# Optimization experiments

Hardware: AMD Instinct MI355X
Metric: run time of the kernel (lower is better)

Reference implementation:

```python
import jax, jax.numpy as jnp
import numpy as np

B, CIN, H, W = 4, 128, 128, 128
CH = CIN // 2          # channels after transpose conv (= 64)
COUT = 64
N2 = (B * 2 * H * 2 * W) // 2  # active sites of x2 (half of fine grid)


def setup_inputs() -> dict:
    key = jax.random.key(0)
    ks = jax.random.split(key, 8)
    n = lambda k, s, sc=1.0: jax.random.normal(k, s, jnp.float32) * sc
    return {
        "x1": n(ks[0], (B, CIN, H, W)),
        "x2_feat": n(ks[1], (N2, CH)),
        "w_up": n(ks[2], (CIN, CH, 2, 2), 0.05),   # torch ConvTranspose2d layout [in, out, kh, kw]
        "b_up": n(ks[3], (CH,), 0.05),
        "w1": n(ks[4], (CH, CH, 3, 3), 0.05),      # torch Conv2d layout [out, in, kh, kw]
        "b1": n(ks[5], (CH,), 0.05),
        "a1": jnp.full((1,), 0.25, jnp.float32),   # nn.PReLU default init
        "w2": n(ks[6], (COUT, CH, 3, 3), 0.05),
        "b2": n(ks[7], (COUT,), 0.05),
        "a2": jnp.full((1,), 0.25, jnp.float32),
    }


def _prelu(x, a):
    return jnp.where(x >= 0, x, a * x)


def _conv3(x, w, b):
    y = jax.lax.conv_general_dilated(x, w, (1, 1), 'SAME',
                                     dimension_numbers=('NCHW', 'OIHW', 'NCHW'))
    return y + b[None, :, None, None]


def reference(x1, x2_feat, w_up, b_up, w1, b1, a1, w2, b2, a2):
    Bn, _, Hn, Wn = x1.shape
    # ConvTranspose2d k=2, s=2 (non-overlapping) as an einsum:
    # up[b,o,2i+p,2j+q] = sum_c x1[b,c,i,j] * w_up[c,o,p,q]
    up = jnp.einsum('bchw,copq->bohpwq', x1, w_up).reshape(Bn, CH, 2 * Hn, 2 * Wn)
    up = up + b_up[None, :, None, None]
    # addspvec: larger tensor keeps its indices; first len(b) feature rows
    # are overwritten by the smaller tensor's features (spconv raster order).
    f = jnp.transpose(up, (0, 2, 3, 1)).reshape(-1, CH)  # [B*2H*2W, CH]
    f = f.at[:x2_feat.shape[0]].set(x2_feat)
    merged = jnp.transpose(f.reshape(Bn, 2 * Hn, 2 * Wn, CH), (0, 3, 1, 2))
    # DoubleConv: (SparseConv2d 3x3 pad1 -> PReLU) x 2 (dense-equivalent)
    h = _prelu(_conv3(merged, w1, b1), a1[0])
    out = _prelu(_conv3(h, w2, b2), a2[0])
    return out
```

## Files before the change

kernel.cpp:

```cpp
#include <hip/hip_runtime.h>

typedef __attribute__((ext_vector_type(8))) short short8;
typedef __attribute__((ext_vector_type(4))) float f32x4;

#define HF 256
#define WF 256

typedef const __attribute__((address_space(1))) void gbl_void;
typedef __attribute__((address_space(3))) void lds_void;

__device__ __forceinline__ ushort f2bf(float f) {
    uint u = __builtin_bit_cast(uint, f);
    u = (u + 0x7FFFu + ((u >> 16) & 1u)) >> 16;
    return (ushort)u;
}
__device__ __forceinline__ uint pack2(float a, float b) {
    return (uint)f2bf(a) | ((uint)f2bf(b) << 16);
}
__device__ __forceinline__ float prelu(float v, float al) { return v >= 0.f ? v : al * v; }

__global__ __launch_bounds__(256) void k_wprep(const float* __restrict__ w1,
                                               const float* __restrict__ w2,
                                               ushort* __restrict__ wT1,
                                               ushort* __restrict__ wT2,
                                               uint4* __restrict__ zeroBuf) {
    if (blockIdx.x == 0 && threadIdx.x < 16)
        zeroBuf[threadIdx.x] = make_uint4(0u, 0u, 0u, 0u);
    int idx = blockIdx.x * 256 + threadIdx.x;
    int tap = idx >> 12;
    int oc  = idx & 4095;
    int src = oc * 9 + tap;
    wT1[idx] = f2bf(w1[src]);
    wT2[idx] = f2bf(w2[src]);
}

__global__ __launch_bounds__(256) void k_wprep_up(const float* __restrict__ wup,
                                                  ushort* __restrict__ wupT) {
    int idx = blockIdx.x * 256 + threadIdx.x;
    int out = idx >> 7;
    int c   = idx & 127;
    int k   = out >> 6;
    int o   = out & 63;
    wupT[idx] = f2bf(wup[c * 256 + o * 4 + k]);
}

__global__ __launch_bounds__(512) void k_upsample_mfma(const float* __restrict__ x1,
                                                       const ushort* __restrict__ wupT,
                                                       const float* __restrict__ bup,
                                                       ushort* __restrict__ upB) {
    __shared__ __align__(16) char lds[81920];

    const int t   = threadIdx.x;
    const int l   = t & 63;
    const int l15 = l & 15;
    const int l4  = l >> 4;
    const int w   = t >> 6;
    const int pg  = w & 3;
    const int oh  = w >> 2;
    const int i   = blockIdx.x >> 1;
    const int j0  = (blockIdx.x & 1) * 64;
    const int z   = blockIdx.y;
    const int gb  = 2 + z;

    {
        const int j  = t & 63;
        const int cg = t >> 6;
        const size_t base = ((size_t)gb * 128) * 16384 + (size_t)i * 128 + j0 + j;
        float xv[16];
#pragma unroll
        for (int r = 0; r < 2; ++r)
#pragma unroll
            for (int cc = 0; cc < 8; ++cc)
                xv[r * 8 + cc] = x1[base + (size_t)(cg * 16 + r * 8 + cc) * 16384];
#pragma unroll
        for (int r = 0; r < 2; ++r) {
            short8 pk;
#pragma unroll
            for (int cc = 0; cc < 8; ++cc) pk[cc] = (short)f2bf(xv[r * 8 + cc]);
            int ad = (j * 256 + (cg * 16 + r * 8) * 2) ^ ((j & 15) << 4);
            *(short8*)(lds + ad) = pk;
        }
    }
    {
        const uint4* src = (const uint4*)wupT;
#pragma unroll
        for (int rep = 0; rep < 8; ++rep) {
            int q   = rep * 512 + t;
            int out = q >> 4, c16 = q & 15;
            int ad  = 16384 + ((out * 256 + c16 * 16) ^ ((out & 15) << 4));
            *(uint4*)(lds + ad) = src[q];
        }
    }
    float bvv[4];
#pragma unroll
    for (int ob = 0; ob < 4; ++ob) bvv[ob] = bup[ob * 16 + l15];
    __syncthreads();

    f32x4 acc[2][4];
#pragma unroll
    for (int kk = 0; kk < 2; ++kk)
#pragma unroll
        for (int ob = 0; ob < 4; ++ob) acc[kk][ob] = (f32x4){0.f, 0.f, 0.f, 0.f};

#pragma unroll
    for (int ks = 0; ks < 4; ++ks) {
        const int cb = ks * 64 + (l4 << 4);
        const int rowA = pg * 16 + l15;
        short8 xfr = *(const short8*)(lds + ((rowA * 256 + cb) ^ ((rowA & 15) << 4)));
#pragma unroll
        for (int kk = 0; kk < 2; ++kk)
#pragma unroll
            for (int ob = 0; ob < 4; ++ob) {
                int out = (oh * 2 + kk) * 64 + ob * 16 + l15;
                short8 wfr = *(const short8*)(lds + 16384 +
                              ((out * 256 + cb) ^ ((out & 15) << 4)));
                acc[kk][ob] = __builtin_amdgcn_mfma_f32_16x16x32_bf16(xfr, wfr, acc[kk][ob], 0, 0, 0);
            }
    }
    __syncthreads();

    ushort* OUT = (ushort*)lds;
#pragma unroll
    for (int kk = 0; kk < 2; ++kk) {
        const int k = oh * 2 + kk, p = k >> 1, q = k & 1;
#pragma unroll
        for (int ob = 0; ob < 4; ++ob) {
            const int o = ob * 16 + l15;
#pragma unroll
            for (int r = 0; r < 4; ++r) {
                int jl = pg * 16 + l4 * 4 + r;
                int x  = 2 * jl + q;
                OUT[(p * 128 + x) * 64 + o] = f2bf(acc[kk][ob][r] + bvv[ob]);
            }
        }
    }
    __syncthreads();

#pragma unroll
    for (int rep = 0; rep < 4; ++rep) {
        int idx = rep * 512 + t;
        int p   = idx >> 10;
        int y   = 2 * i + p;
        uint4 v = *(const uint4*)(lds + idx * 16);
        size_t g = (size_t)(z * HF + y) * 2048 + (size_t)j0 * 16 + (idx & 1023);
        ((uint4*)upB)[g] = v;
    }
}

template<int IN_MODE, int OUT_NHWC>
__global__ __launch_bounds__(512, 1) void k_conv(const float* __restrict__ x2,
                                                 const ushort* __restrict__ upB,
                                                 const ushort* __restrict__ inB,
                                                 const ushort* __restrict__ wT,
                                                 const float* __restrict__ bias,
                                                 const float* __restrict__ alpha,
                                                 const uint4* __restrict__ zeroBuf,
                                                 ushort* __restrict__ outB,
                                                 float* __restrict__ outF) {
    __shared__ __align__(16) ushort inL[5120 * 8];
    __shared__ __align__(16) ushort wL[9 * 64 * 64];

    const int t   = threadIdx.x;
    const int wv  = t >> 6;
    const int l   = t & 63;
    const int l15 = l & 15;
    const int l4  = l >> 4;
    const int x0  = (blockIdx.x & 7) * 32;
    const int y0  = (blockIdx.x >> 3) * 16;
    const int b   = blockIdx.y;

    {
        const char* wTb = (const char*)wT;
#pragma unroll
        for (int rep = 0; rep < 9; ++rep) {
            int d   = rep * 512 + t;
            int tap = d >> 9;
            int dp  = d & 511;
            int s   = (tap << 9) + (dp ^ ((dp >> 3) & 7));
            __builtin_amdgcn_global_load_lds(
                (gbl_void*)(wTb + (size_t)s * 16),
                (lds_void*)((char*)wL + (size_t)((rep << 9) + (wv << 6)) * 16),
                16, 0, 0);
        }
    }

    if (IN_MODE == 1 || b >= 2) {
        const ushort* src0 = (IN_MODE == 1) ? inB : upB;
        const int bb = (IN_MODE == 1) ? b : (b - 2);
#pragma unroll
        for (int rep = 0; rep < 10; ++rep) {
            int d  = rep * 512 + t;
            int r  = d / 272;
            int wi = d - r * 272;
            int wq = wi ^ ((wi >> 3) & 7);
            int x  = wq >> 3, c8 = wq & 7;
            int gy = y0 - 1 + r;
            int gx = x0 - 1 + x;
            const void* g;
            if (d < 4896 && (unsigned)gy < HF && (unsigned)gx < WF) {
                size_t pos = (size_t)(bb * HF + gy) * WF + gx;
                g = (const void*)(src0 + pos * 64 + c8 * 8);
            } else {
                g = (const void*)zeroBuf;
            }
            __builtin_amdgcn_global_load_lds(
                (gbl_void*)g,
                (lds_void*)((char*)inL + (size_t)((rep << 9) + (wv << 6)) * 16),
                16, 0, 0);
        }
    } else {
        for (int q = t; q < 18 * 34 * 8; q += 512) {
            int r   = q / 272;
            int rem = q - r * 272;
            int x   = rem >> 3;
            int c8  = rem & 7;
            int gy = y0 - 1 + r;
            int gx = x0 - 1 + x;
            uint4 v = make_uint4(0u, 0u, 0u, 0u);
            if ((unsigned)gy < HF && (unsigned)gx < WF) {
                size_t pos = (size_t)(b * HF + gy) * WF + gx;
                const float4* s = (const float4*)(x2 + pos * 64 + c8 * 8);
                float4 u0 = s[0], u1 = s[1];
                v = make_uint4(pack2(u0.x, u0.y), pack2(u0.z, u0.w),
                               pack2(u1.x, u1.y), pack2(u1.z, u1.w));
            }
            int ad = (q * 16) ^ ((x & 7) << 4);
            *(uint4*)((char*)inL + ad) = v;
        }
    }
    __syncthreads();

    f32x4 acc[4][4];
#pragma unroll
    for (int m = 0; m < 4; ++m)
#pragma unroll
        for (int nf = 0; nf < 4; ++nf) acc[m][nf] = (f32x4){0.f, 0.f, 0.f, 0.f};

#pragma unroll 1
    for (int tap = 0; tap < 9; ++tap) {
        const int ky = tap / 3;
        const int kx = tap - ky * 3;
        const char* wPage = (const char*)wL + tap * 8192;
#pragma unroll
        for (int ks = 0; ks < 2; ++ks) {
            short8 wfr[4];
#pragma unroll
            for (int nf = 0; nf < 4; ++nf) {
                int o = nf * 16 + l15;
                int ad = (o * 128 + ks * 64 + (l4 << 4)) ^ ((o & 7) << 4);
                wfr[nf] = *(const short8*)(wPage + ad);
            }
#pragma unroll
            for (int m = 0; m < 4; ++m) {
                int ry = wv * 2 + (m >> 1) + ky;
                int xl = (m & 1) * 16 + l15 + kx;
                int ad = ((ry * 34 + xl) * 128 + ks * 64 + (l4 << 4)) ^ ((xl & 7) << 4);
                short8 ifr = *(const short8*)((const char*)inL + ad);
#pragma unroll
                for (int nf = 0; nf < 4; ++nf) {
                    if (OUT_NHWC)
                        acc[m][nf] = __builtin_amdgcn_mfma_f32_16x16x32_bf16(
                            wfr[nf], ifr, acc[m][nf], 0, 0, 0);
                    else
                        acc[m][nf] = __builtin_amdgcn_mfma_f32_16x16x32_bf16(
                            ifr, wfr[nf], acc[m][nf], 0, 0, 0);
                }
            }
        }
    }

    const float al = alpha[0];
    if (OUT_NHWC) {
        float4 bv[4];
#pragma unroll
        for (int nf = 0; nf < 4; ++nf) bv[nf] = *(const float4*)(bias + nf * 16 + (l4 << 2));
#pragma unroll
        for (int m = 0; m < 4; ++m) {
            int y = y0 + wv * 2 + (m >> 1);
            int x = x0 + (m & 1) * 16 + l15;
#pragma unroll
            for (int nf = 0; nf < 4; ++nf) {
                f32x4 v = acc[m][nf];
                uint lo = pack2(prelu(v.x + bv[nf].x, al), prelu(v.y + bv[nf].y, al));
                uint hi = pack2(prelu(v.z + bv[nf].z, al), prelu(v.w + bv[nf].w, al));
                int cb = nf * 16 + (l4 << 2);
                *(uint2*)(outB + ((size_t)(b * HF + y) * WF + x) * 64 + cb) = make_uint2(lo, hi);
            }
        }
    } else {
        float bb[4];
#pragma unroll
        for (int nf = 0; nf < 4; ++nf) bb[nf] = bias[nf * 16 + l15];
#pragma unroll
        for (int m = 0; m < 4; ++m) {
            int y  = y0 + wv * 2 + (m >> 1);
            int xb = x0 + (m & 1) * 16 + (l4 << 2);
#pragma unroll
            for (int nf = 0; nf < 4; ++nf) {
                f32x4 v = acc[m][nf];
                int cout = nf * 16 + l15;
                float4 st;
                st.x = prelu(v.x + bb[nf], al);
                st.y = prelu(v.y + bb[nf], al);
                st.z = prelu(v.z + bb[nf], al);
                st.w = prelu(v.w + bb[nf], al);
                *(float4*)(outF + (((size_t)b * 64 + cout) << 16) + y * WF + xb) = st;
            }
        }
    }
}

extern "C" void kernel_launch(void* const* d_in, const int* in_sizes, int n_in,
                              void* d_out, int out_size, void* d_ws, size_t ws_size,
                              hipStream_t stream) {
    const float* x1  = (const float*)d_in[0];
    const float* x2  = (const float*)d_in[1];
    const float* wup = (const float*)d_in[2];
    const float* bup = (const float*)d_in[3];
    const float* w1  = (const float*)d_in[4];
    const float* b1  = (const float*)d_in[5];
    const float* a1  = (const float*)d_in[6];
    const float* w2  = (const float*)d_in[7];
    const float* b2  = (const float*)d_in[8];
    const float* a2  = (const float*)d_in[9];

    char* ws = (char*)d_ws;
    ushort* upB  = (ushort*)ws;
    ushort* hB   = (ushort*)(ws + (size_t)(16 << 20));
    ushort* wT1  = (ushort*)(ws + (size_t)(48 << 20));
    ushort* wT2  = wT1 + 9 * 64 * 64;
    ushort* wupT = wT2 + 9 * 64 * 64;
    uint4*  zeroBuf = (uint4*)(ws + (size_t)(49 << 20));
    float* out = (float*)d_out;

    k_wprep<<<144, 256, 0, stream>>>(w1, w2, wT1, wT2, zeroBuf);
    k_wprep_up<<<128, 256, 0, stream>>>(wup, wupT);
    k_upsample_mfma<<<dim3(256, 2), 512, 0, stream>>>(x1, wupT, bup, upB);
    k_conv<0, 1><<<dim3(128, 4), 512, 0, stream>>>(x2, upB, nullptr, wT1, b1, a1, zeroBuf, hB, nullptr);
    k_conv<1, 0><<<dim3(128, 4), 512, 0, stream>>>(nullptr, nullptr, hB, wT2, b2, a2, zeroBuf, nullptr, out);
}
```

Measured before the change: 82.52 us.

## Double-buffer conv input tiles across four row sub-tiles per block

Each conv block now covers 32 rows as four 8-row sub-tiles. While one sub-tile is computed from one LDS buffer, the next is staged into a second buffer, so global loads overlap MFMA work and the block's weight load is amortised over more output. The grid is halved to 256 blocks, which on a many-CU device may leave CUs idle, and accumulators per wave shrink to eight.

```diff
diff --git a/kernel.cpp b/kernel.cpp
--- a/kernel.cpp
+++ b/kernel.cpp
@@ -147,7 +147,7 @@
     }
 }
 
-template<int IN_MODE, int OUT_NHWC>
+template<int IN_SPLIT, int OUT_NHWC>
 __global__ __launch_bounds__(512, 1) void k_conv(const float* __restrict__ x2,
                                                  const ushort* __restrict__ upB,
                                                  const ushort* __restrict__ inB,
@@ -157,7 +157,8 @@
                                                  const uint4* __restrict__ zeroBuf,
                                                  ushort* __restrict__ outB,
                                                  float* __restrict__ outF) {
-    __shared__ __align__(16) ushort inL[5120 * 8];
+    __shared__ __align__(16) ushort inLA[2752 * 8];
+    __shared__ __align__(16) ushort inLB[2752 * 8];
     __shared__ __align__(16) ushort wL[9 * 64 * 64];
 
     const int t   = threadIdx.x;
@@ -166,8 +167,12 @@
     const int l15 = l & 15;
     const int l4  = l >> 4;
     const int x0  = (blockIdx.x & 7) * 32;
-    const int y0  = (blockIdx.x >> 3) * 16;
+    const int y0  = (blockIdx.x >> 3) * 32;
     const int b   = blockIdx.y;
+
+    const bool manual = (IN_SPLIT == 1) && (b < 2);
+    const ushort* src = (IN_SPLIT == 1) ? upB : inB;
+    const int bb = (IN_SPLIT == 1) ? (b - 2) : b;
 
     {
         const char* wTb = (const char*)wT;
@@ -184,37 +189,37 @@
         }
     }
 
-    if (IN_MODE == 1 || b >= 2) {
-        const ushort* src0 = (IN_MODE == 1) ? inB : upB;
-        const int bb = (IN_MODE == 1) ? b : (b - 2);
-#pragma unroll
-        for (int rep = 0; rep < 10; ++rep) {
-            int d  = rep * 512 + t;
+    auto stage_async = [&](char* dst, int y0t) {
+#pragma unroll
+        for (int rep = 0; rep < 6; ++rep) {
+            int d = rep * 512 + t;
+            if (d >= 2752) break;
             int r  = d / 272;
             int wi = d - r * 272;
             int wq = wi ^ ((wi >> 3) & 7);
             int x  = wq >> 3, c8 = wq & 7;
-            int gy = y0 - 1 + r;
+            int gy = y0t - 1 + r;
             int gx = x0 - 1 + x;
             const void* g;
-            if (d < 4896 && (unsigned)gy < HF && (unsigned)gx < WF) {
+            if (d < 2720 && (unsigned)gy < HF && (unsigned)gx < WF) {
                 size_t pos = (size_t)(bb * HF + gy) * WF + gx;
-                g = (const void*)(src0 + pos * 64 + c8 * 8);
+                g = (const void*)(src + pos * 64 + c8 * 8);
             } else {
                 g = (const void*)zeroBuf;
             }
             __builtin_amdgcn_global_load_lds(
                 (gbl_void*)g,
-                (lds_void*)((char*)inL + (size_t)((rep << 9) + (wv << 6)) * 16),
+                (lds_void*)(dst + (size_t)((rep << 9) + (wv << 6)) * 16),
                 16, 0, 0);
         }
-    } else {
-        for (int q = t; q < 18 * 34 * 8; q += 512) {
+    };
+    auto stage_manual = [&](char* dst, int y0t) {
+        for (int q = t; q < 2720; q += 512) {
             int r   = q / 272;
             int rem = q - r * 272;
             int x   = rem >> 3;
             int c8  = rem & 7;
-            int gy = y0 - 1 + r;
+            int gy = y0t - 1 + r;
             int gx = x0 - 1 + x;
             uint4 v = make_uint4(0u, 0u, 0u, 0u);
             if ((unsigned)gy < HF && (unsigned)gx < WF) {
@@ -225,88 +230,106 @@
                                pack2(u1.x, u1.y), pack2(u1.z, u1.w));
             }
             int ad = (q * 16) ^ ((x & 7) << 4);
-            *(uint4*)((char*)inL + ad) = v;
-        }
-    }
+            *(uint4*)(dst + ad) = v;
+        }
+    };
+
+    if (manual) stage_manual((char*)inLA, y0);
+    else        stage_async((char*)inLA, y0);
     __syncthreads();
 
-    f32x4 acc[4][4];
-#pragma unroll
-    for (int m = 0; m < 4; ++m)
-#pragma unroll
-        for (int nf = 0; nf < 4; ++nf) acc[m][nf] = (f32x4){0.f, 0.f, 0.f, 0.f};
+    const float al = alpha[0];
+    float4 bv4[4];
+    float  bsc[4];
+#pragma unroll
+    for (int nf = 0; nf < 4; ++nf) {
+        bv4[nf] = *(const float4*)(bias + nf * 16 + (l4 << 2));
+        bsc[nf] = bias[nf * 16 + l15];
+    }
 
 #pragma unroll 1
-    for (int tap = 0; tap < 9; ++tap) {
-        const int ky = tap / 3;
-        const int kx = tap - ky * 3;
-        const char* wPage = (const char*)wL + tap * 8192;
-#pragma unroll
-        for (int ks = 0; ks < 2; ++ks) {
-            short8 wfr[4];
-#pragma unroll
-            for (int nf = 0; nf < 4; ++nf) {
-                int o = nf * 16 + l15;
-                int ad = (o * 128 + ks * 64 + (l4 << 4)) ^ ((o & 7) << 4);
-                wfr[nf] = *(const short8*)(wPage + ad);
-            }
-#pragma unroll
-            for (int m = 0; m < 4; ++m) {
-                int ry = wv * 2 + (m >> 1) + ky;
-                int xl = (m & 1) * 16 + l15 + kx;
-                int ad = ((ry * 34 + xl) * 128 + ks * 64 + (l4 << 4)) ^ ((xl & 7) << 4);
-                short8 ifr = *(const short8*)((const char*)inL + ad);
+    for (int tt = 0; tt < 4; ++tt) {
+        char* cur = (tt & 1) ? (char*)inLB : (char*)inLA;
+        char* nxt = (tt & 1) ? (char*)inLA : (char*)inLB;
+        const int y0t = y0 + tt * 8;
+
+        if (tt < 3) {
+            if (manual) stage_manual(nxt, y0t + 8);
+            else        stage_async(nxt, y0t + 8);
+        }
+
+        f32x4 acc[2][4];
+#pragma unroll
+        for (int m = 0; m < 2; ++m)
+#pragma unroll
+            for (int nf = 0; nf < 4; ++nf) acc[m][nf] = (f32x4){0.f, 0.f, 0.f, 0.f};
+
+#pragma unroll 1
+        for (int tap = 0; tap < 9; ++tap) {
+            const int ky = tap / 3;
+            const int kx = tap - ky * 3;
+            const char* wPage = (const char*)wL + tap * 8192;
+#pragma unroll
+            for (int ks = 0; ks < 2; ++ks) {
+                short8 wfr[4];
 #pragma unroll
                 for (int nf = 0; nf < 4; ++nf) {
-                    if (OUT_NHWC)
-                        acc[m][nf] = __builtin_amdgcn_mfma_f32_16x16x32_bf16(
-                            wfr[nf], ifr, acc[m][nf], 0, 0, 0);
-                    else
-                        acc[m][nf] = __builtin_amdgcn_mfma_f32_16x16x32_bf16(
-                            ifr, wfr[nf], acc[m][nf], 0, 0, 0);
+                    int o = nf * 16 + l15;
+                    int ad = (o * 128 + ks * 64 + (l4 << 4)) ^ ((o & 7) << 4);
+                    wfr[nf] = *(const short8*)(wPage + ad);
                 }
-            }
-        }
-    }
-
-    const float al = alpha[0];
-    if (OUT_NHWC) {
-        float4 bv[4];
-#pragma unroll
-        for (int nf = 0; nf < 4; ++nf) bv[nf] = *(const float4*)(bias + nf * 16 + (l4 << 2));
-#pragma unroll
-        for (int m = 0; m < 4; ++m) {
-            int y = y0 + wv * 2 + (m >> 1);
-            int x = x0 + (m & 1) * 16 + l15;
-#pragma unroll
-            for (int nf = 0; nf < 4; ++nf) {
-                f32x4 v = acc[m][nf];
-                uint lo = pack2(prelu(v.x + bv[nf].x, al), prelu(v.y + bv[nf].y, al));
-                uint hi = pack2(prelu(v.z + bv[nf].z, al), prelu(v.w + bv[nf].w, al));
-                int cb = nf * 16 + (l4 << 2);
-                *(uint2*)(outB + ((size_t)(b * HF + y) * WF + x) * 64 + cb) = make_uint2(lo, hi);
-            }
-        }
-    } else {
-        float bb[4];
-#pragma unroll
-        for (int nf = 0; nf < 4; ++nf) bb[nf] = bias[nf * 16 + l15];
-#pragma unroll
-        for (int m = 0; m < 4; ++m) {
-            int y  = y0 + wv * 2 + (m >> 1);
-            int xb = x0 + (m & 1) * 16 + (l4 << 2);
-#pragma unroll
-            for (int nf = 0; nf < 4; ++nf) {
-                f32x4 v = acc[m][nf];
-                int cout = nf * 16 + l15;
-                float4 st;
-                st.x = prelu(v.x + bb[nf], al);
-                st.y = prelu(v.y + bb[nf], al);
-                st.z = prelu(v.z + bb[nf], al);
-                st.w = prelu(v.w + bb[nf], al);
-                *(float4*)(outF + (((size_t)b * 64 + cout) << 16) + y * WF + xb) = st;
-            }
-        }
+#pragma unroll
+                for (int m = 0; m < 2; ++m) {
+                    int ry = wv + ky;
+                    int xl = m * 16 + l15 + kx;
+                    int ad = ((ry * 34 + xl) * 128 + ks * 64 + (l4 << 4)) ^ ((xl & 7) << 4);
+                    short8 ifr = *(const short8*)(cur + ad);
+#pragma unroll
+                    for (int nf = 0; nf < 4; ++nf) {
+                        if (OUT_NHWC)
+                            acc[m][nf] = __builtin_amdgcn_mfma_f32_16x16x32_bf16(
+                                wfr[nf], ifr, acc[m][nf], 0, 0, 0);
+                        else
+                            acc[m][nf] = __builtin_amdgcn_mfma_f32_16x16x32_bf16(
+                                ifr, wfr[nf], acc[m][nf], 0, 0, 0);
+                    }
+                }
+            }
+        }
+
+        const int y = y0t + wv;
+        if (OUT_NHWC) {
+#pragma unroll
+            for (int m = 0; m < 2; ++m) {
+                int x = x0 + m * 16 + l15;
+#pragma unroll
+                for (int nf = 0; nf < 4; ++nf) {
+                    f32x4 v = acc[m][nf];
+                    uint lo = pack2(prelu(v.x + bv4[nf].x, al), prelu(v.y + bv4[nf].y, al));
+                    uint hi = pack2(prelu(v.z + bv4[nf].z, al), prelu(v.w + bv4[nf].w, al));
+                    int cb = nf * 16 + (l4 << 2);
+                    *(uint2*)(outB + ((size_t)(b * HF + y) * WF + x) * 64 + cb) =
+                        make_uint2(lo, hi);
+                }
+            }
+        } else {
+#pragma unroll
+            for (int m = 0; m < 2; ++m) {
+                int xb = x0 + m * 16 + (l4 << 2);
+#pragma unroll
+                for (int nf = 0; nf < 4; ++nf) {
+                    f32x4 v = acc[m][nf];
+                    int cout = nf * 16 + l15;
+                    float4 st;
+                    st.x = prelu(v.x + bsc[nf], al);
+                    st.y = prelu(v.y + bsc[nf], al);
+                    st.z = prelu(v.z + bsc[nf], al);
+                    st.w = prelu(v.w + bsc[nf], al);
+                    *(float4*)(outF + (((size_t)b * 64 + cout) << 16) + y * WF + xb) = st;
+                }
+            }
+        }
+        __syncthreads();
     }
 }
 
@@ -336,6 +359,6 @@
     k_wprep<<<144, 256, 0, stream>>>(w1, w2, wT1, wT2, zeroBuf);
     k_wprep_up<<<128, 256, 0, stream>>>(wup, wupT);
     k_upsample_mfma<<<dim3(256, 2), 512, 0, stream>>>(x1, wupT, bup, upB);
-    k_conv<0, 1><<<dim3(128, 4), 512, 0, stream>>>(x2, upB, nullptr, wT1, b1, a1, zeroBuf, hB, nullptr);
-    k_conv<1, 0><<<dim3(128, 4), 512, 0, stream>>>(nullptr, nullptr, hB, wT2, b2, a2, zeroBuf, nullptr, out);
-}
+    k_conv<1, 1><<<dim3(64, 4), 512, 0, stream>>>(x2, upB, nullptr, wT1, b1, a1, zeroBuf, hB, nullptr);
+    k_conv<0, 0><<<dim3(64, 4), 512, 0, stream>>>(nullptr, nullptr, hB, wT2, b2, a2, zeroBuf, nullptr, out);
+}
```

New measurement: 82.85 us. No clear change (+0.4%).

## Use 1024-thread conv blocks with one row per wave; merge weight prep kernels

Applied to the files above, without the earlier changes.

The conv kernels now launch 16 waves per block instead of 8, and each wave computes a single output row of 32 pixels instead of two rows, halving per-wave accumulators. The cooperative LDS fills are reindexed for 1024 threads. The aim is more waves in flight per CU to hide LDS and MFMA latency, at the cost of reloading weight fragments across twice as many waves. The two weight-prep kernels are also fused into one launch to save a kernel launch.

```diff
diff --git a/kernel.cpp b/kernel.cpp
--- a/kernel.cpp
+++ b/kernel.cpp
@@ -21,27 +21,28 @@
 
 __global__ __launch_bounds__(256) void k_wprep(const float* __restrict__ w1,
                                                const float* __restrict__ w2,
+                                               const float* __restrict__ wup,
                                                ushort* __restrict__ wT1,
                                                ushort* __restrict__ wT2,
+                                               ushort* __restrict__ wupT,
                                                uint4* __restrict__ zeroBuf) {
+    int idx = blockIdx.x * 256 + threadIdx.x;
     if (blockIdx.x == 0 && threadIdx.x < 16)
         zeroBuf[threadIdx.x] = make_uint4(0u, 0u, 0u, 0u);
-    int idx = blockIdx.x * 256 + threadIdx.x;
-    int tap = idx >> 12;
-    int oc  = idx & 4095;
-    int src = oc * 9 + tap;
-    wT1[idx] = f2bf(w1[src]);
-    wT2[idx] = f2bf(w2[src]);
-}
-
-__global__ __launch_bounds__(256) void k_wprep_up(const float* __restrict__ wup,
-                                                  ushort* __restrict__ wupT) {
-    int idx = blockIdx.x * 256 + threadIdx.x;
-    int out = idx >> 7;
-    int c   = idx & 127;
-    int k   = out >> 6;
-    int o   = out & 63;
-    wupT[idx] = f2bf(wup[c * 256 + o * 4 + k]);
+    if (idx < 36864) {
+        int tap = idx >> 12;
+        int oc  = idx & 4095;
+        int src = oc * 9 + tap;
+        wT1[idx] = f2bf(w1[src]);
+        wT2[idx] = f2bf(w2[src]);
+    }
+    if (idx < 32768) {
+        int out = idx >> 7;
+        int c   = idx & 127;
+        int k   = out >> 6;
+        int o   = out & 63;
+        wupT[idx] = f2bf(wup[c * 256 + o * 4 + k]);
+    }
 }
 
 __global__ __launch_bounds__(512) void k_upsample_mfma(const float* __restrict__ x1,
@@ -148,15 +149,15 @@
 }
 
 template<int IN_MODE, int OUT_NHWC>
-__global__ __launch_bounds__(512, 1) void k_conv(const float* __restrict__ x2,
-                                                 const ushort* __restrict__ upB,
-                                                 const ushort* __restrict__ inB,
-                                                 const ushort* __restrict__ wT,
-                                                 const float* __restrict__ bias,
-                                                 const float* __restrict__ alpha,
-                                                 const uint4* __restrict__ zeroBuf,
-                                                 ushort* __restrict__ outB,
-                                                 float* __restrict__ outF) {
+__global__ __launch_bounds__(1024, 1) void k_conv(const float* __restrict__ x2,
+                                                  const ushort* __restrict__ upB,
+                                                  const ushort* __restrict__ inB,
+                                                  const ushort* __restrict__ wT,
+                                                  const float* __restrict__ bias,
+                                                  const float* __restrict__ alpha,
+                                                  const uint4* __restrict__ zeroBuf,
+                                                  ushort* __restrict__ outB,
+                                                  float* __restrict__ outF) {
     __shared__ __align__(16) ushort inL[5120 * 8];
     __shared__ __align__(16) ushort wL[9 * 64 * 64];
 
@@ -172,14 +173,24 @@
     {
         const char* wTb = (const char*)wT;
 #pragma unroll
-        for (int rep = 0; rep < 9; ++rep) {
-            int d   = rep * 512 + t;
+        for (int rep = 0; rep < 4; ++rep) {
+            int d   = rep * 1024 + t;
             int tap = d >> 9;
             int dp  = d & 511;
             int s   = (tap << 9) + (dp ^ ((dp >> 3) & 7));
             __builtin_amdgcn_global_load_lds(
                 (gbl_void*)(wTb + (size_t)s * 16),
-                (lds_void*)((char*)wL + (size_t)((rep << 9) + (wv << 6)) * 16),
+                (lds_void*)((char*)wL + (size_t)((rep << 10) + (wv << 6)) * 16),
+                16, 0, 0);
+        }
+        if (wv < 8) {
+            int d   = 4096 + (wv << 6) + l;
+            int tap = d >> 9;
+            int dp  = d & 511;
+            int s   = (tap << 9) + (dp ^ ((dp >> 3) & 7));
+            __builtin_amdgcn_global_load_lds(
+                (gbl_void*)(wTb + (size_t)s * 16),
+                (lds_void*)((char*)wL + (size_t)(4096 + (wv << 6)) * 16),
                 16, 0, 0);
         }
     }
@@ -188,8 +199,8 @@
         const ushort* src0 = (IN_MODE == 1) ? inB : upB;
         const int bb = (IN_MODE == 1) ? b : (b - 2);
 #pragma unroll
-        for (int rep = 0; rep < 10; ++rep) {
-            int d  = rep * 512 + t;
+        for (int rep = 0; rep < 5; ++rep) {
+            int d  = rep * 1024 + t;
             int r  = d / 272;
             int wi = d - r * 272;
             int wq = wi ^ ((wi >> 3) & 7);
@@ -205,11 +216,11 @@
             }
             __builtin_amdgcn_global_load_lds(
                 (gbl_void*)g,
-                (lds_void*)((char*)inL + (size_t)((rep << 9) + (wv << 6)) * 16),
+                (lds_void*)((char*)inL + (size_t)((rep << 10) + (wv << 6)) * 16),
                 16, 0, 0);
         }
     } else {
-        for (int q = t; q < 18 * 34 * 8; q += 512) {
+        for (int q = t; q < 18 * 34 * 8; q += 1024) {
             int r   = q / 272;
             int rem = q - r * 272;
             int x   = rem >> 3;
@@ -230,9 +241,9 @@
     }
     __syncthreads();
 
-    f32x4 acc[4][4];
-#pragma unroll
-    for (int m = 0; m < 4; ++m)
+    f32x4 acc[2][4];
+#pragma unroll
+    for (int m = 0; m < 2; ++m)
 #pragma unroll
         for (int nf = 0; nf < 4; ++nf) acc[m][nf] = (f32x4){0.f, 0.f, 0.f, 0.f};
 
@@ -251,9 +262,9 @@
                 wfr[nf] = *(const short8*)(wPage + ad);
             }
 #pragma unroll
-            for (int m = 0; m < 4; ++m) {
-                int ry = wv * 2 + (m >> 1) + ky;
-                int xl = (m & 1) * 16 + l15 + kx;
+            for (int m = 0; m < 2; ++m) {
+                int ry = wv + ky;
+                int xl = m * 16 + l15 + kx;
                 int ad = ((ry * 34 + xl) * 128 + ks * 64 + (l4 << 4)) ^ ((xl & 7) << 4);
                 short8 ifr = *(const short8*)((const char*)inL + ad);
 #pragma unroll
@@ -270,14 +281,14 @@
     }
 
     const float al = alpha[0];
+    const int y = y0 + wv;
     if (OUT_NHWC) {
         float4 bv[4];
 #pragma unroll
         for (int nf = 0; nf < 4; ++nf) bv[nf] = *(const float4*)(bias + nf * 16 + (l4 << 2));
 #pragma unroll
-        for (int m = 0; m < 4; ++m) {
-            int y = y0 + wv * 2 + (m >> 1);
-            int x = x0 + (m & 1) * 16 + l15;
+        for (int m = 0; m < 2; ++m) {
+            int x = x0 + m * 16 + l15;
 #pragma unroll
             for (int nf = 0; nf < 4; ++nf) {
                 f32x4 v = acc[m][nf];
@@ -292,9 +303,8 @@
 #pragma unroll
         for (int nf = 0; nf < 4; ++nf) bb[nf] = bias[nf * 16 + l15];
 #pragma unroll
-        for (int m = 0; m < 4; ++m) {
-            int y  = y0 + wv * 2 + (m >> 1);
-            int xb = x0 + (m & 1) * 16 + (l4 << 2);
+        for (int m = 0; m < 2; ++m) {
+            int xb = x0 + m * 16 + (l4 << 2);
 #pragma unroll
             for (int nf = 0; nf < 4; ++nf) {
                 f32x4 v = acc[m][nf];
@@ -333,9 +343,8 @@
     uint4*  zeroBuf = (uint4*)(ws + (size_t)(49 << 20));
     float* out = (float*)d_out;
 
-    k_wprep<<<144, 256, 0, stream>>>(w1, w2, wT1, wT2, zeroBuf);
-    k_wprep_up<<<128, 256, 0, stream>>>(wup, wupT);
+    k_wprep<<<144, 256, 0, stream>>>(w1, w2, wup, wT1, wT2, wupT, zeroBuf);
     k_upsample_mfma<<<dim3(256, 2), 512, 0, stream>>>(x1, wupT, bup, upB);
-    k_conv<0, 1><<<dim3(128, 4), 512, 0, stream>>>(x2, upB, nullptr, wT1, b1, a1, zeroBuf, hB, nullptr);
-    k_conv<1, 0><<<dim3(128, 4), 512, 0, stream>>>(nullptr, nullptr, hB, wT2, b2, a2, zeroBuf, nullptr, out);
-}
+    k_conv<0, 1><<<dim3(128, 4), 1024, 0, stream>>>(x2, upB, nullptr, wT1, b1, a1, zeroBuf, hB, nullptr);
+    k_conv<1, 0><<<dim3(128, 4), 1024, 0, stream>>>(nullptr, nullptr, hB, wT2, b2, a2, zeroBuf, nullptr, out);
+}
```

Result: faster. 80.10 us (median of 2 runs) (-2.9%).
